# Kernel optimization log

Hardware: AMD Instinct MI355X
Metric: run time of the kernel (lower is better)

The kernel has to match this reference:

```python
import jax, jax.numpy as jnp
import numpy as np

IN_F = 256
OUT_F = 256
HYPER = 128
BATCH = 4096


def setup_inputs() -> dict:
    key = jax.random.key(0)
    ks = jax.random.split(key, 9)
    s_in = 1.0 / np.sqrt(IN_F)
    s_h = 1.0 / np.sqrt(HYPER)
    x = jax.random.normal(ks[0], (BATCH, IN_F), dtype=jnp.float32)
    # weight_gen: Linear(in, hyper) -> ReLU -> Linear(hyper, in*out)
    W1g = jax.random.uniform(ks[1], (IN_F, HYPER), jnp.float32, -s_in, s_in)
    b1g = jax.random.uniform(ks[2], (HYPER,), jnp.float32, -s_in, s_in)
    W2g = jax.random.uniform(ks[3], (HYPER, IN_F * OUT_F), jnp.float32, -s_h, s_h)
    b2g = jax.random.uniform(ks[4], (IN_F * OUT_F,), jnp.float32, -s_h, s_h)
    # bias_gen: Linear(in, hyper) -> ReLU -> Linear(hyper, out)
    W1b = jax.random.uniform(ks[5], (IN_F, HYPER), jnp.float32, -s_in, s_in)
    b1b = jax.random.uniform(ks[6], (HYPER,), jnp.float32, -s_in, s_in)
    W2b = jax.random.uniform(ks[7], (HYPER, OUT_F), jnp.float32, -s_h, s_h)
    b2b = jax.random.uniform(ks[8], (OUT_F,), jnp.float32, -s_h, s_h)
    return {"x": x, "W1g": W1g, "b1g": b1g, "W2g": W2g, "b2g": b2g,
            "W1b": W1b, "b1b": b1b, "W2b": W2b, "b2b": b2b}


def reference(x, W1g, b1g, W2g, b2g, W1b, b1b, W2b, b2b):
    B = x.shape[0]
    # generate per-sample weights [B, out, in]
    hg = jax.nn.relu(x @ W1g + b1g)                      # [B, hyper]
    weights = (hg @ W2g + b2g).reshape(B, OUT_F, IN_F)   # [B, out, in]
    # generate per-sample bias [B, out]
    hb = jax.nn.relu(x @ W1b + b1b)                      # [B, hyper]
    bias = hb @ W2b + b2b                                # [B, out]
    # batched matvec: bmm(weights, x[...,None]) + bias
    out = jnp.einsum('boi,bi->bo', weights, x) + bias    # [B, out]
    return out
```

## Files before the change

kernel.cpp:

```cpp
#include <hip/hip_runtime.h>

#define AS1 __attribute__((address_space(1)))
#define AS3 __attribute__((address_space(3)))

typedef short short8 __attribute__((ext_vector_type(8)));
typedef float f32x16 __attribute__((ext_vector_type(16)));
typedef unsigned short ushort4v __attribute__((ext_vector_type(4)));

#define BATCH 4096
#define IN_F 256
#define OUT_F 256
#define HYP 128
#define HX 129
#define KP (HX * IN_F)
#define NGEMMP 32
#define NVB 516

__device__ __forceinline__ float bf2f(unsigned short u) {
  unsigned v = ((unsigned)u) << 16;
  float f;
  __builtin_memcpy(&f, &v, 4);
  return f;
}
__device__ __forceinline__ unsigned short f2bf(float f) {
  unsigned u;
  __builtin_memcpy(&u, &f, 4);
  unsigned r = u + 0x7fffu + ((u >> 16) & 1u);
  return (unsigned short)(r >> 16);
}

__device__ __forceinline__ void gld_lds16(const unsigned short* g, unsigned short* s) {
  __builtin_amdgcn_global_load_lds((const AS1 unsigned int*)g, (AS3 unsigned int*)s, 16, 0, 0);
}

__global__ __launch_bounds__(256) void k_trans(const float* __restrict__ W1g,
                                               const float* __restrict__ W1b,
                                               const float* __restrict__ W2b,
                                               unsigned short* __restrict__ W1T,
                                               unsigned short* __restrict__ W2bT) {
  const int t = threadIdx.x, b = blockIdx.x;
  if (b < 64) {
#pragma unroll
    for (int i = 0; i < 4; ++i) {
      const int e = b * 1024 + i * 256 + t;
      const int n = e >> 8, k = e & 255;
      const float v = (n < HYP) ? W1g[k * HYP + n] : W1b[k * HYP + (n - HYP)];
      W1T[e] = f2bf(v);
    }
  } else {
#pragma unroll
    for (int i = 0; i < 4; ++i) {
      const int e = (b - 64) * 1024 + i * 256 + t;
      const int o = e >> 7, h = e & 127;
      W2bT[e] = f2bf(W2b[h * OUT_F + o]);
    }
  }
}

__global__ __launch_bounds__(512) void k_prep(
    const float* __restrict__ x,
    const float* __restrict__ b1g, const float* __restrict__ b1b,
    const float* __restrict__ b2b,
    const float* __restrict__ W2g, const float* __restrict__ b2g,
    const unsigned short* __restrict__ W1T, const unsigned short* __restrict__ W2bT,
    unsigned short* __restrict__ Vb, unsigned short* __restrict__ hgbT,
    unsigned short* __restrict__ xb, float* __restrict__ out) {
  __shared__ __align__(16) unsigned short xS[128 * 256];
  __shared__ __align__(16) unsigned short hbS[128 * 128];
  const int t = threadIdx.x;

  if (blockIdx.x >= NGEMMP) {
    const int base = (blockIdx.x - NGEMMP) * 2048 + t;
#pragma unroll
    for (int it = 0; it < 4; ++it) {
      const int cid = base + it * 512;
      const int ic = cid & 31;
      const int pair = cid >> 5;
      const int h = pair % HX;
      const int o = pair / HX;
      const float* src = (h < HYP) ? (W2g + (size_t)h * (OUT_F * IN_F) + o * IN_F + ic * 8)
                                   : (b2g + o * IN_F + ic * 8);
      const float4 v0 = ((const float4*)src)[0];
      const float4 v1 = ((const float4*)src)[1];
      uint4 pk;
      pk.x = (unsigned)f2bf(v0.x) | ((unsigned)f2bf(v0.y) << 16);
      pk.y = (unsigned)f2bf(v0.z) | ((unsigned)f2bf(v0.w) << 16);
      pk.z = (unsigned)f2bf(v1.x) | ((unsigned)f2bf(v1.y) << 16);
      pk.w = (unsigned)f2bf(v1.z) | ((unsigned)f2bf(v1.w) << 16);
      *(uint4*)(Vb + (size_t)o * KP + h * IN_F + ic * 8) = pk;
    }
    return;
  }

  const int lane = t & 63;
  const int w = t >> 6;
  const int l31 = lane & 31;
  const int hi = lane >> 5;
  const int m0 = blockIdx.x * 128;

#pragma unroll
  for (int j = 0; j < 16; ++j) {
    const int row = j * 8 + w;
    const float4 v = *(const float4*)(x + (size_t)(m0 + row) * IN_F + lane * 4);
    uint2 pk;
    pk.x = (unsigned)f2bf(v.x) | ((unsigned)f2bf(v.y) << 16);
    pk.y = (unsigned)f2bf(v.z) | ((unsigned)f2bf(v.w) << 16);
    *(uint2*)(xb + (size_t)(m0 + row) * IN_F + lane * 4) = pk;
    const int ch = lane >> 1, half = lane & 1;
    *(uint2*)(&xS[row * 256 + ((ch ^ (row & 31))) * 8 + half * 4]) = pk;
  }
  __syncthreads();

  const int hA = w * 32 + l31;
  uint4 af[16];
#pragma unroll
  for (int kt = 0; kt < 16; ++kt)
    af[kt] = *(const uint4*)(W1T + (size_t)hA * 256 + kt * 16 + hi * 8);

  f32x16 zv;
#pragma unroll
  for (int i = 0; i < 16; ++i) zv[i] = 0.0f;
  f32x16 d0 = zv, d1 = zv, d2 = zv, d3 = zv;
#pragma unroll
  for (int kt = 0; kt < 16; ++kt) {
    const int pos = (kt * 2 + hi) ^ l31;
    const short8 a = __builtin_bit_cast(short8, af[kt]);
#define G1STEP(CS, DD)                                                        \
    {                                                                         \
      const short8 bfrg = *(const short8*)(&xS[(CS * 32 + l31) * 256 + pos * 8]); \
      DD = __builtin_amdgcn_mfma_f32_32x32x16_bf16(a, bfrg, DD, 0, 0, 0);     \
    }
    G1STEP(0, d0) G1STEP(1, d1) G1STEP(2, d2) G1STEP(3, d3)
#undef G1STEP
  }

  if (w < 4) {
    float4 bq[4];
#pragma unroll
    for (int q = 0; q < 4; ++q)
      bq[q] = *(const float4*)(b1g + w * 32 + q * 8 + hi * 4);
#define EPI_G(CS, DD)                                                         \
    {                                                                         \
      const int mcol = m0 + CS * 32 + l31;                                    \
      _Pragma("unroll")                                                       \
      for (int g = 0; g < 16; ++g) {                                          \
        const int h = w * 32 + (g & 3) + 8 * (g >> 2) + 4 * hi;               \
        float v = DD[g] + ((const float*)&bq[g >> 2])[g & 3];                 \
        v = v > 0.f ? v : 0.f;                                                \
        hgbT[(size_t)h * BATCH + mcol] = f2bf(v);                             \
      }                                                                       \
    }
    EPI_G(0, d0) EPI_G(1, d1) EPI_G(2, d2) EPI_G(3, d3)
#undef EPI_G
  } else {
    float4 bq[4];
#pragma unroll
    for (int q = 0; q < 4; ++q)
      bq[q] = *(const float4*)(b1b + (w - 4) * 32 + q * 8 + hi * 4);
#define EPI_B(CS, DD)                                                         \
    {                                                                         \
      const int m = CS * 32 + l31;                                            \
      _Pragma("unroll")                                                       \
      for (int q = 0; q < 4; ++q) {                                           \
        float v0 = DD[q * 4 + 0] + ((const float*)&bq[q])[0];                 \
        float v1 = DD[q * 4 + 1] + ((const float*)&bq[q])[1];                 \
        float v2 = DD[q * 4 + 2] + ((const float*)&bq[q])[2];                 \
        float v3 = DD[q * 4 + 3] + ((const float*)&bq[q])[3];                 \
        v0 = v0 > 0.f ? v0 : 0.f; v1 = v1 > 0.f ? v1 : 0.f;                   \
        v2 = v2 > 0.f ? v2 : 0.f; v3 = v3 > 0.f ? v3 : 0.f;                   \
        uint2 pk;                                                             \
        pk.x = (unsigned)f2bf(v0) | ((unsigned)f2bf(v1) << 16);               \
        pk.y = (unsigned)f2bf(v2) | ((unsigned)f2bf(v3) << 16);               \
        const int chunk = (w - 4) * 4 + q;                                    \
        *(uint2*)(&hbS[m * 128 + ((chunk ^ (m & 15))) * 8 + hi * 4]) = pk;    \
      }                                                                       \
    }
    EPI_B(0, d0) EPI_B(1, d1) EPI_B(2, d2) EPI_B(3, d3)
#undef EPI_B
  }
  __syncthreads();

  const int msub = w & 3, oh = w >> 2;
  const int mA = msub * 32 + l31;
  f32x16 e0 = zv, e1 = zv, e2 = zv, e3 = zv;
#pragma unroll
  for (int kt = 0; kt < 8; ++kt) {
    const int pos = (kt * 2 + hi) ^ (mA & 15);
    const short8 a = *(const short8*)(&hbS[mA * 128 + pos * 8]);
#define G2STEP(OS, EE)                                                        \
    {                                                                         \
      const int orow = oh * 128 + OS * 32 + l31;                              \
      const short8 bb = *(const short8*)(W2bT + (size_t)orow * 128 + kt * 16 + hi * 8); \
      EE = __builtin_amdgcn_mfma_f32_32x32x16_bf16(a, bb, EE, 0, 0, 0);       \
    }
    G2STEP(0, e0) G2STEP(1, e1) G2STEP(2, e2) G2STEP(3, e3)
#undef G2STEP
  }
#define EPI2(OS, EE)                                                          \
  {                                                                           \
    const int o = oh * 128 + OS * 32 + l31;                                   \
    const float bo = b2b[o];                                                  \
    _Pragma("unroll")                                                         \
    for (int g = 0; g < 16; ++g) {                                            \
      const int m = m0 + msub * 32 + (g & 3) + 8 * (g >> 2) + 4 * hi;         \
      out[(size_t)m * OUT_F + o] = EE[g] + bo;                                \
    }                                                                         \
  }
  EPI2(0, e0) EPI2(1, e1) EPI2(2, e2) EPI2(3, e3)
#undef EPI2
}

__global__ __launch_bounds__(512, 2) void k_gemm(const unsigned short* __restrict__ Vb,
                                                 const unsigned short* __restrict__ hgbT,
                                                 const unsigned short* __restrict__ xb,
                                                 float* __restrict__ out) {
  __shared__ __align__(16) unsigned short Bl[2][64 * 256];
  __shared__ __align__(16) unsigned short hgs[33 * 256];
  const int tid = threadIdx.x;
  const int lane = tid & 63;
  const int wave = tid >> 6;
  const int l31 = lane & 31;
  const int hi = lane >> 5;
  const int wm = wave & 3;
  const int wo = wave >> 2;

  const int bid = blockIdx.x;
  const int c = bid & 7;
  const int t2 = bid >> 3;
  const int xm = t2 & 15;
  const int g8 = t2 >> 4;
  const int grp = c + 8 * g8;
  const int yo = grp & 3;
  const int z = grp >> 2;

  const int m0 = xm * 256;
  const int o0 = yo * 64;
  const int hBeg = (z * HX) >> 2;
  const int hEnd = ((z + 1) * HX) >> 2;
  const int nh = hEnd - hBeg;

  for (int idx = tid; idx < nh * 256; idx += 512) {
    const int hl = idx >> 8;
    const int hh = hBeg + hl;
    hgs[idx] = (hh == HYP) ? (unsigned short)0x3F80
                           : hgbT[(size_t)hh * BATCH + m0 + (idx & 255)];
  }

  const int mrow0 = m0 + wm * 64 + l31;
  const int mrow1 = mrow0 + 32;
  uint4 xf0[16], xf1[16];
#pragma unroll
  for (int j = 0; j < 16; ++j) {
    xf0[j] = *(const uint4*)(xb + (size_t)mrow0 * IN_F + j * 16 + hi * 8);
    xf1[j] = *(const uint4*)(xb + (size_t)mrow1 * IN_F + j * 16 + hi * 8);
  }

  const int nB = tid >> 5;
  const int p = tid & 31;
  const int cs = p ^ (nB & 7);
  const unsigned short* gsrc = Vb + (size_t)(o0 + nB) * KP + cs * 8 + (size_t)hBeg * IN_F;

  f32x16 zv;
#pragma unroll
  for (int i = 0; i < 16; ++i) zv[i] = 0.0f;
  f32x16 acc0 = zv, acc1 = zv;
  f32x16 ah0 = zv, ah1 = zv;

#pragma unroll
  for (int j = 0; j < 4; ++j)
    gld_lds16(gsrc + (size_t)j * 16 * KP, &Bl[0][(tid + 512 * j) * 8]);
  __syncthreads();

  for (int r = 0; r < nh; ++r) {
    const int buf = r & 1;
    if (r + 1 < nh) {
      const unsigned short* gs = gsrc + (size_t)(r + 1) * IN_F;
#pragma unroll
      for (int j = 0; j < 4; ++j)
        gld_lds16(gs + (size_t)j * 16 * KP, &Bl[buf ^ 1][(tid + 512 * j) * 8]);
    }
    const unsigned short* bp = &Bl[buf][0];
    const int rowb = wo * 32 + l31;
#pragma unroll
    for (int ic = 0; ic < 4; ++ic) {
#pragma unroll
      for (int t = 0; t < 4; ++t) {
        const int c0 = ic * 8 + t * 2 + hi;
        const int pr = c0 ^ (l31 & 7);
        const short8 b0 = *(const short8*)(bp + rowb * 256 + pr * 8);
        const short8 a0 = __builtin_bit_cast(short8, xf0[ic * 4 + t]);
        const short8 a1 = __builtin_bit_cast(short8, xf1[ic * 4 + t]);
        ah0 = __builtin_amdgcn_mfma_f32_32x32x16_bf16(a0, b0, ah0, 0, 0, 0);
        ah1 = __builtin_amdgcn_mfma_f32_32x32x16_bf16(a1, b0, ah1, 0, 0, 0);
      }
    }
#pragma unroll
    for (int q = 0; q < 4; ++q) {
      const ushort4v v0 = *(const ushort4v*)&hgs[r * 256 + wm * 64 + 4 * hi + q * 8];
      const ushort4v v1 = *(const ushort4v*)&hgs[r * 256 + wm * 64 + 32 + 4 * hi + q * 8];
#pragma unroll
      for (int e = 0; e < 4; ++e) {
        acc0[q * 4 + e] += bf2f(v0[e]) * ah0[q * 4 + e];
        acc1[q * 4 + e] += bf2f(v1[e]) * ah1[q * 4 + e];
      }
    }
    ah0 = zv; ah1 = zv;
    __syncthreads();
  }

  const int mb = m0 + wm * 64 + 4 * hi;
  const int col = o0 + wo * 32 + l31;
#pragma unroll
  for (int g = 0; g < 16; ++g) {
    const int row0 = mb + (g & 3) + 8 * (g >> 2);
    atomicAdd(&out[(size_t)row0 * OUT_F + col], acc0[g]);
    atomicAdd(&out[(size_t)(row0 + 32) * OUT_F + col], acc1[g]);
  }
}

extern "C" void kernel_launch(void* const* d_in, const int* in_sizes, int n_in,
                              void* d_out, int out_size, void* d_ws, size_t ws_size,
                              hipStream_t stream) {
  const float* x = (const float*)d_in[0];
  const float* W1g = (const float*)d_in[1];
  const float* b1g = (const float*)d_in[2];
  const float* W2g = (const float*)d_in[3];
  const float* b2g = (const float*)d_in[4];
  const float* W1b = (const float*)d_in[5];
  const float* b1b = (const float*)d_in[6];
  const float* W2b = (const float*)d_in[7];
  const float* b2b = (const float*)d_in[8];
  float* out = (float*)d_out;

  char* ws = (char*)d_ws;
  const size_t szV = (size_t)OUT_F * KP * 2;
  const size_t szHg = (size_t)HYP * BATCH * 2;
  const size_t szXb = (size_t)BATCH * IN_F * 2;
  const size_t szW1T = (size_t)256 * 256 * 2;
  unsigned short* Vb = (unsigned short*)ws;
  unsigned short* hgbT = (unsigned short*)(ws + szV);
  unsigned short* xb = (unsigned short*)(ws + szV + szHg);
  unsigned short* W1T = (unsigned short*)(ws + szV + szHg + szXb);
  unsigned short* W2bT = (unsigned short*)(ws + szV + szHg + szXb + szW1T);

  hipLaunchKernelGGL(k_trans, dim3(96), dim3(256), 0, stream, W1g, W1b, W2b, W1T, W2bT);
  hipLaunchKernelGGL(k_prep, dim3(NGEMMP + NVB), dim3(512), 0, stream,
                     x, b1g, b1b, b2b, W2g, b2g, W1T, W2bT, Vb, hgbT, xb, out);
  hipLaunchKernelGGL(k_gemm, dim3(256), dim3(512), 0, stream, Vb, hgbT, xb, out);
}
```

Measured before the change: 186.2 us.

## Fuse prep and GEMM into one cooperative kernel with triple-buffered loads

Merges the prep kernel (x conversion, hidden-layer GEMMs, bias output, W2g to bf16 repack) and the main GEMM into a single cooperative launch of 256 blocks, separated by a grid-wide sync. The prep work is redistributed: 128 blocks each handle 32 batch rows, and the other 128 blocks run a grid-stride loop over the weight repack. The GEMM stage moves from double to triple buffering of the Vb tiles, with explicit vmcnt waits and raw barriers so loads stay in flight across iterations. This removes one kernel launch boundary and its tail, but adds the cost of the grid sync, needs all blocks co-resident at 2 blocks per CU, and leaves the repack on only half the grid.

```diff
diff --git a/kernel.cpp b/kernel.cpp
--- a/kernel.cpp
+++ b/kernel.cpp
@@ -1,4 +1,7 @@
 #include <hip/hip_runtime.h>
+#include <hip/hip_cooperative_groups.h>
+
+namespace cg = cooperative_groups;
 
 #define AS1 __attribute__((address_space(1)))
 #define AS3 __attribute__((address_space(3)))
@@ -13,8 +16,7 @@
 #define HYP 128
 #define HX 129
 #define KP (HX * IN_F)
-#define NGEMMP 32
-#define NVB 516
+#define TILE (64 * 256)
 
 __device__ __forceinline__ float bf2f(unsigned short u) {
   unsigned v = ((unsigned)u) << 16;
@@ -57,7 +59,7 @@
   }
 }
 
-__global__ __launch_bounds__(512) void k_prep(
+__global__ __launch_bounds__(512, 2) void k_all(
     const float* __restrict__ x,
     const float* __restrict__ b1g, const float* __restrict__ b1b,
     const float* __restrict__ b2b,
@@ -65,15 +67,105 @@
     const unsigned short* __restrict__ W1T, const unsigned short* __restrict__ W2bT,
     unsigned short* __restrict__ Vb, unsigned short* __restrict__ hgbT,
     unsigned short* __restrict__ xb, float* __restrict__ out) {
-  __shared__ __align__(16) unsigned short xS[128 * 256];
-  __shared__ __align__(16) unsigned short hbS[128 * 128];
+  __shared__ __align__(16) unsigned short SMEM[3 * TILE + 33 * 256];
   const int t = threadIdx.x;
-
-  if (blockIdx.x >= NGEMMP) {
-    const int base = (blockIdx.x - NGEMMP) * 2048 + t;
-#pragma unroll
-    for (int it = 0; it < 4; ++it) {
-      const int cid = base + it * 512;
+  const int lane = t & 63;
+  const int w = t >> 6;
+  const int l31 = lane & 31;
+  const int hi = lane >> 5;
+  const int bid = blockIdx.x;
+
+  f32x16 zv;
+#pragma unroll
+  for (int i = 0; i < 16; ++i) zv[i] = 0.0f;
+
+  if (bid < 128) {
+    unsigned short* xS = SMEM;
+    unsigned short* hbS = SMEM + 32 * 256;
+    const int m0 = bid * 32;
+
+#pragma unroll
+    for (int j = 0; j < 4; ++j) {
+      const int row = j * 8 + w;
+      const float4 v = *(const float4*)(x + (size_t)(m0 + row) * IN_F + lane * 4);
+      uint2 pk;
+      pk.x = (unsigned)f2bf(v.x) | ((unsigned)f2bf(v.y) << 16);
+      pk.y = (unsigned)f2bf(v.z) | ((unsigned)f2bf(v.w) << 16);
+      *(uint2*)(xb + (size_t)(m0 + row) * IN_F + lane * 4) = pk;
+      const int ch = lane >> 1, half = lane & 1;
+      *(uint2*)(&xS[row * 256 + (ch ^ row) * 8 + half * 4]) = pk;
+    }
+    __syncthreads();
+
+    const int hA = w * 32 + l31;
+    uint4 af[16];
+#pragma unroll
+    for (int kt = 0; kt < 16; ++kt)
+      af[kt] = *(const uint4*)(W1T + (size_t)hA * 256 + kt * 16 + hi * 8);
+    f32x16 d = zv;
+#pragma unroll
+    for (int kt = 0; kt < 16; ++kt) {
+      const int pos = (kt * 2 + hi) ^ l31;
+      const short8 a = __builtin_bit_cast(short8, af[kt]);
+      const short8 b = *(const short8*)(&xS[l31 * 256 + pos * 8]);
+      d = __builtin_amdgcn_mfma_f32_32x32x16_bf16(a, b, d, 0, 0, 0);
+    }
+
+    if (w < 4) {
+      float4 bq[4];
+#pragma unroll
+      for (int q = 0; q < 4; ++q)
+        bq[q] = *(const float4*)(b1g + w * 32 + q * 8 + hi * 4);
+      const int mcol = m0 + l31;
+#pragma unroll
+      for (int g = 0; g < 16; ++g) {
+        const int h = w * 32 + (g & 3) + 8 * (g >> 2) + 4 * hi;
+        float v = d[g] + ((const float*)&bq[g >> 2])[g & 3];
+        v = v > 0.f ? v : 0.f;
+        hgbT[(size_t)h * BATCH + mcol] = f2bf(v);
+      }
+    } else {
+      float4 bq[4];
+#pragma unroll
+      for (int q = 0; q < 4; ++q)
+        bq[q] = *(const float4*)(b1b + (w - 4) * 32 + q * 8 + hi * 4);
+      const int m = l31;
+#pragma unroll
+      for (int q = 0; q < 4; ++q) {
+        float v0 = d[q * 4 + 0] + ((const float*)&bq[q])[0];
+        float v1 = d[q * 4 + 1] + ((const float*)&bq[q])[1];
+        float v2 = d[q * 4 + 2] + ((const float*)&bq[q])[2];
+        float v3 = d[q * 4 + 3] + ((const float*)&bq[q])[3];
+        v0 = v0 > 0.f ? v0 : 0.f; v1 = v1 > 0.f ? v1 : 0.f;
+        v2 = v2 > 0.f ? v2 : 0.f; v3 = v3 > 0.f ? v3 : 0.f;
+        uint2 pk;
+        pk.x = (unsigned)f2bf(v0) | ((unsigned)f2bf(v1) << 16);
+        pk.y = (unsigned)f2bf(v2) | ((unsigned)f2bf(v3) << 16);
+        const int chunk = (w - 4) * 4 + q;
+        *(uint2*)(&hbS[m * 128 + ((chunk ^ (m & 15))) * 8 + hi * 4]) = pk;
+      }
+    }
+    __syncthreads();
+
+    f32x16 e = zv;
+#pragma unroll
+    for (int kt = 0; kt < 8; ++kt) {
+      const int pos = (kt * 2 + hi) ^ (l31 & 15);
+      const short8 a = *(const short8*)(&hbS[l31 * 128 + pos * 8]);
+      const short8 b = *(const short8*)(W2bT + (size_t)(w * 32 + l31) * 128 + kt * 16 + hi * 8);
+      e = __builtin_amdgcn_mfma_f32_32x32x16_bf16(a, b, e, 0, 0, 0);
+    }
+    const int o = w * 32 + l31;
+    const float bo = b2b[o];
+#pragma unroll
+    for (int g = 0; g < 16; ++g) {
+      const int m = m0 + (g & 3) + 8 * (g >> 2) + 4 * hi;
+      out[(size_t)m * OUT_F + o] = e[g] + bo;
+    }
+  } else {
+    const int vb = bid - 128;
+    const int NC = 256 * HX * 32;
+    for (int cid = vb * 512 + t; cid < NC; cid += 128 * 512) {
       const int ic = cid & 31;
       const int pair = cid >> 5;
       const int h = pair % HX;
@@ -89,232 +181,113 @@
       pk.w = (unsigned)f2bf(v1.z) | ((unsigned)f2bf(v1.w) << 16);
       *(uint4*)(Vb + (size_t)o * KP + h * IN_F + ic * 8) = pk;
     }
-    return;
   }
 
-  const int lane = t & 63;
-  const int w = t >> 6;
-  const int l31 = lane & 31;
-  const int hi = lane >> 5;
-  const int m0 = blockIdx.x * 128;
-
-#pragma unroll
-  for (int j = 0; j < 16; ++j) {
-    const int row = j * 8 + w;
-    const float4 v = *(const float4*)(x + (size_t)(m0 + row) * IN_F + lane * 4);
-    uint2 pk;
-    pk.x = (unsigned)f2bf(v.x) | ((unsigned)f2bf(v.y) << 16);
-    pk.y = (unsigned)f2bf(v.z) | ((unsigned)f2bf(v.w) << 16);
-    *(uint2*)(xb + (size_t)(m0 + row) * IN_F + lane * 4) = pk;
-    const int ch = lane >> 1, half = lane & 1;
-    *(uint2*)(&xS[row * 256 + ((ch ^ (row & 31))) * 8 + half * 4]) = pk;
-  }
-  __syncthreads();
-
-  const int hA = w * 32 + l31;
-  uint4 af[16];
-#pragma unroll
-  for (int kt = 0; kt < 16; ++kt)
-    af[kt] = *(const uint4*)(W1T + (size_t)hA * 256 + kt * 16 + hi * 8);
-
-  f32x16 zv;
-#pragma unroll
-  for (int i = 0; i < 16; ++i) zv[i] = 0.0f;
-  f32x16 d0 = zv, d1 = zv, d2 = zv, d3 = zv;
-#pragma unroll
-  for (int kt = 0; kt < 16; ++kt) {
-    const int pos = (kt * 2 + hi) ^ l31;
-    const short8 a = __builtin_bit_cast(short8, af[kt]);
-#define G1STEP(CS, DD)                                                        \
-    {                                                                         \
-      const short8 bfrg = *(const short8*)(&xS[(CS * 32 + l31) * 256 + pos * 8]); \
-      DD = __builtin_amdgcn_mfma_f32_32x32x16_bf16(a, bfrg, DD, 0, 0, 0);     \
-    }
-    G1STEP(0, d0) G1STEP(1, d1) G1STEP(2, d2) G1STEP(3, d3)
-#undef G1STEP
-  }
-
-  if (w < 4) {
-    float4 bq[4];
-#pragma unroll
-    for (int q = 0; q < 4; ++q)
-      bq[q] = *(const float4*)(b1g + w * 32 + q * 8 + hi * 4);
-#define EPI_G(CS, DD)                                                         \
-    {                                                                         \
-      const int mcol = m0 + CS * 32 + l31;                                    \
-      _Pragma("unroll")                                                       \
-      for (int g = 0; g < 16; ++g) {                                          \
-        const int h = w * 32 + (g & 3) + 8 * (g >> 2) + 4 * hi;               \
-        float v = DD[g] + ((const float*)&bq[g >> 2])[g & 3];                 \
-        v = v > 0.f ? v : 0.f;                                                \
-        hgbT[(size_t)h * BATCH + mcol] = f2bf(v);                             \
-      }                                                                       \
-    }
-    EPI_G(0, d0) EPI_G(1, d1) EPI_G(2, d2) EPI_G(3, d3)
-#undef EPI_G
-  } else {
-    float4 bq[4];
-#pragma unroll
-    for (int q = 0; q < 4; ++q)
-      bq[q] = *(const float4*)(b1b + (w - 4) * 32 + q * 8 + hi * 4);
-#define EPI_B(CS, DD)                                                         \
-    {                                                                         \
-      const int m = CS * 32 + l31;                                            \
-      _Pragma("unroll")                                                       \
-      for (int q = 0; q < 4; ++q) {                                           \
-        float v0 = DD[q * 4 + 0] + ((const float*)&bq[q])[0];                 \
-        float v1 = DD[q * 4 + 1] + ((const float*)&bq[q])[1];                 \
-        float v2 = DD[q * 4 + 2] + ((const float*)&bq[q])[2];                 \
-        float v3 = DD[q * 4 + 3] + ((const float*)&bq[q])[3];                 \
-        v0 = v0 > 0.f ? v0 : 0.f; v1 = v1 > 0.f ? v1 : 0.f;                   \
-        v2 = v2 > 0.f ? v2 : 0.f; v3 = v3 > 0.f ? v3 : 0.f;                   \
-        uint2 pk;                                                             \
-        pk.x = (unsigned)f2bf(v0) | ((unsigned)f2bf(v1) << 16);               \
-        pk.y = (unsigned)f2bf(v2) | ((unsigned)f2bf(v3) << 16);               \
-        const int chunk = (w - 4) * 4 + q;                                    \
-        *(uint2*)(&hbS[m * 128 + ((chunk ^ (m & 15))) * 8 + hi * 4]) = pk;    \
-      }                                                                       \
-    }
-    EPI_B(0, d0) EPI_B(1, d1) EPI_B(2, d2) EPI_B(3, d3)
-#undef EPI_B
-  }
-  __syncthreads();
-
-  const int msub = w & 3, oh = w >> 2;
-  const int mA = msub * 32 + l31;
-  f32x16 e0 = zv, e1 = zv, e2 = zv, e3 = zv;
-#pragma unroll
-  for (int kt = 0; kt < 8; ++kt) {
-    const int pos = (kt * 2 + hi) ^ (mA & 15);
-    const short8 a = *(const short8*)(&hbS[mA * 128 + pos * 8]);
-#define G2STEP(OS, EE)                                                        \
-    {                                                                         \
-      const int orow = oh * 128 + OS * 32 + l31;                              \
-      const short8 bb = *(const short8*)(W2bT + (size_t)orow * 128 + kt * 16 + hi * 8); \
-      EE = __builtin_amdgcn_mfma_f32_32x32x16_bf16(a, bb, EE, 0, 0, 0);       \
-    }
-    G2STEP(0, e0) G2STEP(1, e1) G2STEP(2, e2) G2STEP(3, e3)
-#undef G2STEP
-  }
-#define EPI2(OS, EE)                                                          \
-  {                                                                           \
-    const int o = oh * 128 + OS * 32 + l31;                                   \
-    const float bo = b2b[o];                                                  \
-    _Pragma("unroll")                                                         \
-    for (int g = 0; g < 16; ++g) {                                            \
-      const int m = m0 + msub * 32 + (g & 3) + 8 * (g >> 2) + 4 * hi;         \
-      out[(size_t)m * OUT_F + o] = EE[g] + bo;                                \
-    }                                                                         \
-  }
-  EPI2(0, e0) EPI2(1, e1) EPI2(2, e2) EPI2(3, e3)
-#undef EPI2
-}
-
-__global__ __launch_bounds__(512, 2) void k_gemm(const unsigned short* __restrict__ Vb,
-                                                 const unsigned short* __restrict__ hgbT,
-                                                 const unsigned short* __restrict__ xb,
-                                                 float* __restrict__ out) {
-  __shared__ __align__(16) unsigned short Bl[2][64 * 256];
-  __shared__ __align__(16) unsigned short hgs[33 * 256];
-  const int tid = threadIdx.x;
-  const int lane = tid & 63;
-  const int wave = tid >> 6;
-  const int l31 = lane & 31;
-  const int hi = lane >> 5;
-  const int wm = wave & 3;
-  const int wo = wave >> 2;
-
-  const int bid = blockIdx.x;
-  const int c = bid & 7;
-  const int t2 = bid >> 3;
-  const int xm = t2 & 15;
-  const int g8 = t2 >> 4;
-  const int grp = c + 8 * g8;
-  const int yo = grp & 3;
-  const int z = grp >> 2;
-
-  const int m0 = xm * 256;
-  const int o0 = yo * 64;
-  const int hBeg = (z * HX) >> 2;
-  const int hEnd = ((z + 1) * HX) >> 2;
-  const int nh = hEnd - hBeg;
-
-  for (int idx = tid; idx < nh * 256; idx += 512) {
-    const int hl = idx >> 8;
-    const int hh = hBeg + hl;
-    hgs[idx] = (hh == HYP) ? (unsigned short)0x3F80
-                           : hgbT[(size_t)hh * BATCH + m0 + (idx & 255)];
-  }
-
-  const int mrow0 = m0 + wm * 64 + l31;
-  const int mrow1 = mrow0 + 32;
-  uint4 xf0[16], xf1[16];
-#pragma unroll
-  for (int j = 0; j < 16; ++j) {
-    xf0[j] = *(const uint4*)(xb + (size_t)mrow0 * IN_F + j * 16 + hi * 8);
-    xf1[j] = *(const uint4*)(xb + (size_t)mrow1 * IN_F + j * 16 + hi * 8);
-  }
-
-  const int nB = tid >> 5;
-  const int p = tid & 31;
-  const int cs = p ^ (nB & 7);
-  const unsigned short* gsrc = Vb + (size_t)(o0 + nB) * KP + cs * 8 + (size_t)hBeg * IN_F;
-
-  f32x16 zv;
-#pragma unroll
-  for (int i = 0; i < 16; ++i) zv[i] = 0.0f;
-  f32x16 acc0 = zv, acc1 = zv;
-  f32x16 ah0 = zv, ah1 = zv;
-
-#pragma unroll
-  for (int j = 0; j < 4; ++j)
-    gld_lds16(gsrc + (size_t)j * 16 * KP, &Bl[0][(tid + 512 * j) * 8]);
-  __syncthreads();
-
-  for (int r = 0; r < nh; ++r) {
-    const int buf = r & 1;
-    if (r + 1 < nh) {
-      const unsigned short* gs = gsrc + (size_t)(r + 1) * IN_F;
-#pragma unroll
-      for (int j = 0; j < 4; ++j)
-        gld_lds16(gs + (size_t)j * 16 * KP, &Bl[buf ^ 1][(tid + 512 * j) * 8]);
-    }
-    const unsigned short* bp = &Bl[buf][0];
-    const int rowb = wo * 32 + l31;
-#pragma unroll
-    for (int ic = 0; ic < 4; ++ic) {
-#pragma unroll
-      for (int t = 0; t < 4; ++t) {
-        const int c0 = ic * 8 + t * 2 + hi;
-        const int pr = c0 ^ (l31 & 7);
-        const short8 b0 = *(const short8*)(bp + rowb * 256 + pr * 8);
-        const short8 a0 = __builtin_bit_cast(short8, xf0[ic * 4 + t]);
-        const short8 a1 = __builtin_bit_cast(short8, xf1[ic * 4 + t]);
-        ah0 = __builtin_amdgcn_mfma_f32_32x32x16_bf16(a0, b0, ah0, 0, 0, 0);
-        ah1 = __builtin_amdgcn_mfma_f32_32x32x16_bf16(a1, b0, ah1, 0, 0, 0);
-      }
-    }
-#pragma unroll
-    for (int q = 0; q < 4; ++q) {
-      const ushort4v v0 = *(const ushort4v*)&hgs[r * 256 + wm * 64 + 4 * hi + q * 8];
-      const ushort4v v1 = *(const ushort4v*)&hgs[r * 256 + wm * 64 + 32 + 4 * hi + q * 8];
-#pragma unroll
-      for (int e = 0; e < 4; ++e) {
-        acc0[q * 4 + e] += bf2f(v0[e]) * ah0[q * 4 + e];
-        acc1[q * 4 + e] += bf2f(v1[e]) * ah1[q * 4 + e];
-      }
-    }
-    ah0 = zv; ah1 = zv;
-    __syncthreads();
-  }
-
-  const int mb = m0 + wm * 64 + 4 * hi;
-  const int col = o0 + wo * 32 + l31;
-#pragma unroll
-  for (int g = 0; g < 16; ++g) {
-    const int row0 = mb + (g & 3) + 8 * (g >> 2);
-    atomicAdd(&out[(size_t)row0 * OUT_F + col], acc0[g]);
-    atomicAdd(&out[(size_t)(row0 + 32) * OUT_F + col], acc1[g]);
+  cg::this_grid().sync();
+
+  {
+    unsigned short* Bl = SMEM;
+    unsigned short* hgs = SMEM + 3 * TILE;
+
+    const int c = bid & 7;
+    const int t2 = bid >> 3;
+    const int xm = t2 & 15;
+    const int g8 = t2 >> 4;
+    const int grp = c + 8 * g8;
+    const int yo = grp & 3;
+    const int z = grp >> 2;
+
+    const int m0 = xm * 256;
+    const int o0 = yo * 64;
+    const int hBeg = (z * HX) >> 2;
+    const int hEnd = ((z + 1) * HX) >> 2;
+    const int nh = hEnd - hBeg;
+    const int wm = w & 3;
+    const int wo = w >> 2;
+
+    for (int idx = t; idx < nh * 256; idx += 512) {
+      const int hl = idx >> 8;
+      const int hh = hBeg + hl;
+      hgs[idx] = (hh == HYP) ? (unsigned short)0x3F80
+                             : hgbT[(size_t)hh * BATCH + m0 + (idx & 255)];
+    }
+
+    const int mrow0 = m0 + wm * 64 + l31;
+    const int mrow1 = mrow0 + 32;
+    uint4 xf0[16], xf1[16];
+#pragma unroll
+    for (int j = 0; j < 16; ++j) {
+      xf0[j] = *(const uint4*)(xb + (size_t)mrow0 * IN_F + j * 16 + hi * 8);
+      xf1[j] = *(const uint4*)(xb + (size_t)mrow1 * IN_F + j * 16 + hi * 8);
+    }
+
+    const int nB = t >> 5;
+    const int p = t & 31;
+    const int cs = p ^ (nB & 7);
+    const unsigned short* gsrc = Vb + (size_t)(o0 + nB) * KP + cs * 8 + (size_t)hBeg * IN_F;
+
+    f32x16 acc0 = zv, acc1 = zv, ah0 = zv, ah1 = zv;
+
+#pragma unroll
+    for (int j = 0; j < 4; ++j)
+      gld_lds16(gsrc + (size_t)j * 16 * KP, &Bl[(t + 512 * j) * 8]);
+#pragma unroll
+    for (int j = 0; j < 4; ++j)
+      gld_lds16(gsrc + IN_F + (size_t)j * 16 * KP, &Bl[TILE + (t + 512 * j) * 8]);
+    asm volatile("s_waitcnt vmcnt(4)" ::: "memory");
+    asm volatile("s_waitcnt lgkmcnt(0)" ::: "memory");
+    __builtin_amdgcn_s_barrier();
+
+    for (int r = 0; r < nh; ++r) {
+      if (r + 2 < nh) {
+        const unsigned short* gs = gsrc + (size_t)(r + 2) * IN_F;
+        unsigned short* dst = &Bl[((r + 2) % 3) * TILE];
+#pragma unroll
+        for (int j = 0; j < 4; ++j)
+          gld_lds16(gs + (size_t)j * 16 * KP, dst + (t + 512 * j) * 8);
+      }
+      const unsigned short* bp = &Bl[(r % 3) * TILE];
+      const int rowb = wo * 32 + l31;
+#pragma unroll
+      for (int ic = 0; ic < 4; ++ic) {
+#pragma unroll
+        for (int tt = 0; tt < 4; ++tt) {
+          const int c0 = ic * 8 + tt * 2 + hi;
+          const int pr = c0 ^ (l31 & 7);
+          const short8 b0 = *(const short8*)(bp + rowb * 256 + pr * 8);
+          const short8 a0 = __builtin_bit_cast(short8, xf0[ic * 4 + tt]);
+          const short8 a1 = __builtin_bit_cast(short8, xf1[ic * 4 + tt]);
+          ah0 = __builtin_amdgcn_mfma_f32_32x32x16_bf16(a0, b0, ah0, 0, 0, 0);
+          ah1 = __builtin_amdgcn_mfma_f32_32x32x16_bf16(a1, b0, ah1, 0, 0, 0);
+        }
+      }
+#pragma unroll
+      for (int q = 0; q < 4; ++q) {
+        const ushort4v v0 = *(const ushort4v*)&hgs[r * 256 + wm * 64 + 4 * hi + q * 8];
+        const ushort4v v1 = *(const ushort4v*)&hgs[r * 256 + wm * 64 + 32 + 4 * hi + q * 8];
+#pragma unroll
+        for (int e = 0; e < 4; ++e) {
+          acc0[q * 4 + e] += bf2f(v0[e]) * ah0[q * 4 + e];
+          acc1[q * 4 + e] += bf2f(v1[e]) * ah1[q * 4 + e];
+        }
+      }
+      ah0 = zv; ah1 = zv;
+      if (r + 1 < nh) {
+        if (r + 2 < nh) asm volatile("s_waitcnt vmcnt(4)" ::: "memory");
+        else            asm volatile("s_waitcnt vmcnt(0)" ::: "memory");
+        asm volatile("s_waitcnt lgkmcnt(0)" ::: "memory");
+        __builtin_amdgcn_s_barrier();
+      }
+    }
+
+    const int mb = m0 + wm * 64 + 4 * hi;
+    const int col = o0 + wo * 32 + l31;
+#pragma unroll
+    for (int g = 0; g < 16; ++g) {
+      const int row0 = mb + (g & 3) + 8 * (g >> 2);
+      atomicAdd(&out[(size_t)row0 * OUT_F + col], acc0[g]);
+      atomicAdd(&out[(size_t)(row0 + 32) * OUT_F + col], acc1[g]);
+    }
   }
 }
 
@@ -344,7 +317,10 @@
   unsigned short* W2bT = (unsigned short*)(ws + szV + szHg + szXb + szW1T);
 
   hipLaunchKernelGGL(k_trans, dim3(96), dim3(256), 0, stream, W1g, W1b, W2b, W1T, W2bT);
-  hipLaunchKernelGGL(k_prep, dim3(NGEMMP + NVB), dim3(512), 0, stream,
-                     x, b1g, b1b, b2b, W2g, b2g, W1T, W2bT, Vb, hgbT, xb, out);
-  hipLaunchKernelGGL(k_gemm, dim3(256), dim3(512), 0, stream, Vb, hgbT, xb, out);
-}
+
+  void* args[] = {(void*)&x,   (void*)&b1g, (void*)&b1b, (void*)&b2b,
+                  (void*)&W2g, (void*)&b2g, (void*)&W1T, (void*)&W2bT,
+                  (void*)&Vb,  (void*)&hgbT, (void*)&xb, (void*)&out};
+  hipLaunchCooperativeKernel(reinterpret_cast<void*>(&k_all), dim3(256), dim3(512),
+                             args, 0, stream);
+}
```

Result: slower. 233.2 us (+25.2%).
